# Performance work log

Measured on AMD Instinct MI355X. Metric: run time of the kernel, lower is better.

## Reference

```python
import jax, jax.numpy as jnp
import numpy as np

B, S, D, H, DH, SD = 4, 512, 768, 12, 64, 30
ALPHA, BETA = 1.0, 1.0


def setup_inputs() -> dict:
    root = jax.random.key(0)
    ks = jax.random.split(root, 16)
    n = lambda k, sh: jax.random.normal(k, sh, dtype=jnp.float32)
    w = lambda k, sh: 0.02 * jax.random.normal(k, sh, dtype=jnp.float32)
    return {
        "key": n(ks[0], (B, S, D)),
        "value": n(ks[1], (B, S, D)),
        "query": n(ks[2], (B, S, D)),
        "structure": n(ks[3], (B, S, S, SD)),
        "mask": jax.random.randint(ks[4], (B, S, S), 0, 2).astype(bool),
        "Wq": w(ks[5], (D, D)), "bq": jnp.zeros((D,), jnp.float32),
        "Wk": w(ks[6], (D, D)), "bk": jnp.zeros((D,), jnp.float32),
        "Wv": w(ks[7], (D, D)), "bv": jnp.zeros((D,), jnp.float32),
        "Wsk": w(ks[8], (SD, DH)), "bsk": jnp.zeros((DH,), jnp.float32),
        "Wsv": w(ks[9], (SD, DH)), "bsv": jnp.zeros((DH,), jnp.float32),
        "Wo": w(ks[10], (D, D)), "bo": jnp.zeros((D,), jnp.float32),
    }


def reference(key, value, query, structure, mask,
              Wq, bq, Wk, bk, Wv, bv, Wsk, bsk, Wsv, bsv, Wo, bo):
    # shape: [B,S,D] -> [B,H,S,DH]
    def proj(x, W, b):
        return (x @ W + b).reshape(B, -1, H, DH).transpose(0, 2, 1, 3)

    q = proj(query, Wq, bq) / np.float32(np.sqrt(DH))  # scale applied before both score terms
    k = proj(key, Wk, bk)
    v = proj(value, Wv, bv)

    sk = structure @ Wsk + bsk  # [B,Q,K,DH] relative-structure keys
    sv = structure @ Wsv + bsv  # [B,Q,K,DH] relative-structure values

    scores = jnp.einsum('bhqd,bhkd->bhqk', q, k)
    scores = scores + ALPHA * jnp.einsum('bhqd,bqkd->bhqk', q, sk)
    scores = jnp.where(mask[:, None, :, :], jnp.float32(-1e18), scores)

    attn = jax.nn.softmax(scores, axis=-1)  # dropout p=0 -> identity

    ctx = jnp.einsum('bhqk,bhkd->bhqd', attn, v)
    ctx = ctx + BETA * jnp.einsum('bhqk,bqkd->bhqd', attn, sv)
    ctx = ctx.transpose(0, 2, 1, 3).reshape(B, S, D)

    output = ctx @ Wo + bo
    top_attn = attn[:, 0]  # [B,Q,K]
    return output, top_attn
```

## Files before the change

### kernel.cpp

```cpp
#include <hip/hip_runtime.h>
#include <hip/hip_bf16.h>

typedef unsigned int uint32_ty;

typedef float  nfloat2 __attribute__((ext_vector_type(2)));
typedef float  nfloat4 __attribute__((ext_vector_type(4)));
typedef int    nint4   __attribute__((ext_vector_type(4)));
typedef short  bf16x8  __attribute__((ext_vector_type(8)));
typedef float  f32x4   __attribute__((ext_vector_type(4)));
typedef unsigned short ushort4n __attribute__((ext_vector_type(4)));

#define BB 4
#define SS 512
#define DD 768
#define HH 12
#define DHH 64
#define SDD 30

#define LP 520

__device__ __forceinline__ float bfu(unsigned short u) {
    return __uint_as_float(((uint32_ty)u) << 16);
}
__device__ __forceinline__ unsigned short tobf(float f) {
    return __bfloat16_as_ushort(__float2bfloat16(f));
}
__device__ __forceinline__ void unp8(uint4 u, float* t) {
    t[0] = __uint_as_float(u.x << 16);
    t[1] = __uint_as_float(u.x & 0xFFFF0000u);
    t[2] = __uint_as_float(u.y << 16);
    t[3] = __uint_as_float(u.y & 0xFFFF0000u);
    t[4] = __uint_as_float(u.z << 16);
    t[5] = __uint_as_float(u.z & 0xFFFF0000u);
    t[6] = __uint_as_float(u.w << 16);
    t[7] = __uint_as_float(u.w & 0xFFFF0000u);
}
__device__ __forceinline__ void unp4(uint2 u, float* t) {
    t[0] = __uint_as_float(u.x << 16);
    t[1] = __uint_as_float(u.x & 0xFFFF0000u);
    t[2] = __uint_as_float(u.y << 16);
    t[3] = __uint_as_float(u.y & 0xFFFF0000u);
}

#define MBM 64
#define MBN 64
#define MBK 64
#define LDK 72

__global__ __launch_bounds__(256) void gemm_proj3(
    const float* __restrict__ Xq, const float* __restrict__ Xk, const float* __restrict__ Xv,
    const float* __restrict__ Wq, const float* __restrict__ Wk, const float* __restrict__ Wv,
    const float* __restrict__ bq, const float* __restrict__ bk, const float* __restrict__ bv,
    float* __restrict__ oq, unsigned short* __restrict__ okT, unsigned short* __restrict__ ov)
{
    __shared__ unsigned short As[MBM][LDK];
    __shared__ unsigned short Bs[MBN][LDK];
    int z = blockIdx.z;
    const float* X = (z == 0) ? Xq : (z == 1) ? Xk : Xv;
    const float* W = (z == 0) ? Wq : (z == 1) ? Wk : Wv;
    const float* bias = (z == 0) ? bq : (z == 1) ? bk : bv;

    int tid = threadIdx.x;
    int lane = tid & 63, wave = tid >> 6;
    int m0 = blockIdx.y * MBM, n0 = blockIdx.x * MBN;
    int wm = (wave >> 1) * 32, wn = (wave & 1) * 32;
    int fr = lane & 15, fq = lane >> 4;

    f32x4 acc[2][2];
#pragma unroll
    for (int i = 0; i < 2; i++)
#pragma unroll
        for (int j = 0; j < 2; j++) acc[i][j] = (f32x4){0.f, 0.f, 0.f, 0.f};

    for (int k0 = 0; k0 < DD; k0 += MBK) {
#pragma unroll
        for (int rep = 0; rep < 4; rep++) {
            int i = tid + 256 * rep;
            int r = i >> 4, c4 = i & 15;
            float4 xv = *(const float4*)(X + (size_t)(m0 + r) * DD + k0 + 4 * c4);
            ushort4n pk = {tobf(xv.x), tobf(xv.y), tobf(xv.z), tobf(xv.w)};
            *(ushort4n*)&As[r][4 * c4] = pk;
        }
#pragma unroll
        for (int rep = 0; rep < 4; rep++) {
            int i = tid + 256 * rep;
            int r = i >> 4, c4 = i & 15;
            float4 wv = *(const float4*)(W + (size_t)(k0 + r) * DD + n0 + 4 * c4);
            Bs[4 * c4 + 0][r] = tobf(wv.x);
            Bs[4 * c4 + 1][r] = tobf(wv.y);
            Bs[4 * c4 + 2][r] = tobf(wv.z);
            Bs[4 * c4 + 3][r] = tobf(wv.w);
        }
        __syncthreads();
#pragma unroll
        for (int ks = 0; ks < 2; ks++) {
            bf16x8 a0 = *(bf16x8*)&As[wm + fr][ks * 32 + fq * 8];
            bf16x8 a1 = *(bf16x8*)&As[wm + 16 + fr][ks * 32 + fq * 8];
            bf16x8 b0 = *(bf16x8*)&Bs[wn + fr][ks * 32 + fq * 8];
            bf16x8 b1 = *(bf16x8*)&Bs[wn + 16 + fr][ks * 32 + fq * 8];
            acc[0][0] = __builtin_amdgcn_mfma_f32_16x16x32_bf16(a0, b0, acc[0][0], 0, 0, 0);
            acc[0][1] = __builtin_amdgcn_mfma_f32_16x16x32_bf16(a0, b1, acc[0][1], 0, 0, 0);
            acc[1][0] = __builtin_amdgcn_mfma_f32_16x16x32_bf16(a1, b0, acc[1][0], 0, 0, 0);
            acc[1][1] = __builtin_amdgcn_mfma_f32_16x16x32_bf16(a1, b1, acc[1][1], 0, 0, 0);
        }
        __syncthreads();
    }

#pragma unroll
    for (int i = 0; i < 2; i++) {
#pragma unroll
        for (int j = 0; j < 2; j++) {
            int n = n0 + wn + 16 * j + fr;
            int h = n >> 6, d = n & 63;
            float bn = bias[n];
            int mbase = m0 + wm + 16 * i + fq * 4;
            int b = mbase >> 9, sbase = mbase & 511;
            if (z == 1) {
                ushort4n pk;
#pragma unroll
                for (int r = 0; r < 4; r++) pk[r] = tobf(acc[i][j][r] + bn);
                *(ushort4n*)(okT + ((((size_t)b * HH + h) * DHH + d) * SS + sbase)) = pk;
            } else if (z == 0) {
#pragma unroll
                for (int r = 0; r < 4; r++)
                    oq[((((size_t)b * HH + h) * SS + sbase + r) * DHH + d)] =
                        (acc[i][j][r] + bn) * 0.125f;
            } else {
#pragma unroll
                for (int r = 0; r < 4; r++)
                    ov[((((size_t)b * HH + h) * SS + sbase + r) * DHH + d)] =
                        tobf(acc[i][j][r] + bn);
            }
        }
    }
}

#define TM 64
#define TN 64
#define TKK 32

__global__ __launch_bounds__(256) void gemm_out(
    const float* __restrict__ Xf, const float* __restrict__ W,
    const float* __restrict__ bias, float* __restrict__ out)
{
    __shared__ float As[TKK][TM + 4];
    __shared__ float Bs[TKK][TN + 4];
    int tx = threadIdx.x, ty = threadIdx.y;
    int tid = ty * 16 + tx;
    int m0 = blockIdx.y * TM;
    int n0 = blockIdx.x * TN;
    float acc[4][4] = {};
    for (int k0 = 0; k0 < DD; k0 += TKK) {
#pragma unroll
        for (int rep = 0; rep < 2; rep++) {
            int f = tid + 256 * rep;
            int r = f >> 3, c = f & 7;
            float4 xv = *(const float4*)(Xf + (size_t)(m0 + r) * DD + k0 + 4 * c);
            As[4 * c + 0][r] = xv.x; As[4 * c + 1][r] = xv.y;
            As[4 * c + 2][r] = xv.z; As[4 * c + 3][r] = xv.w;
        }
#pragma unroll
        for (int rep = 0; rep < 2; rep++) {
            int f = tid + 256 * rep;
            int r = f >> 4, c = f & 15;
            float4 wv = *(const float4*)(W + (size_t)(k0 + r) * DD + n0 + 4 * c);
            *(float4*)&Bs[r][4 * c] = wv;
        }
        __syncthreads();
#pragma unroll 8
        for (int kk = 0; kk < TKK; kk++) {
            float4 av = *(float4*)&As[kk][ty * 4];
            float4 bv4 = *(float4*)&Bs[kk][tx * 4];
            float a[4] = {av.x, av.y, av.z, av.w};
            float bb[4] = {bv4.x, bv4.y, bv4.z, bv4.w};
#pragma unroll
            for (int i = 0; i < 4; i++)
#pragma unroll
                for (int j = 0; j < 4; j++) acc[i][j] += a[i] * bb[j];
        }
        __syncthreads();
    }
#pragma unroll
    for (int i = 0; i < 4; i++) {
        int m = m0 + ty * 4 + i;
#pragma unroll
        for (int j = 0; j < 4; j++) {
            int n = n0 + tx * 4 + j;
            out[(size_t)m * DD + n] = acc[i][j] + bias[n];
        }
    }
}

__global__ __launch_bounds__(256) void attn_fused(
    const float* __restrict__ q,
    const unsigned short* __restrict__ kT,
    const unsigned short* __restrict__ v,
    const float* __restrict__ structure,
    const int* __restrict__ mask,
    const float* __restrict__ Wsk,
    const float* __restrict__ bsk,
    const float* __restrict__ Wsv,
    const float* __restrict__ bsv,
    float* __restrict__ ctx,
    float* __restrict__ top_attn)
{
    __shared__ float qs[HH][DHH];
    __shared__ unsigned short stT[SDD][LP];
    __shared__ float qt_s[HH][SDD];
    __shared__ float qb_s[HH];
    __shared__ float astr_s[HH][SDD];
    __shared__ unsigned short at[HH][LP];

    int tid = threadIdx.x;
    int lane = tid & 63, wave = tid >> 6;

    int blk = blockIdx.x;
    int xcd = blk & 7;
    int b = xcd >> 1;
    int qp = ((xcd & 1) << 8) | (blk >> 3);

    for (int i = tid; i < HH * DHH; i += 256) {
        int h = i >> 6, d = i & 63;
        qs[h][d] = q[(((size_t)b * HH + h) * SS + qp) * DHH + d];
    }
    {
        const float* srow = structure + ((size_t)b * SS + qp) * (size_t)(SS * SDD);
        for (int k = tid; k < SS; k += 256) {
            const nfloat2* rp = (const nfloat2*)(srow + (size_t)k * SDD);
#pragma unroll
            for (int w = 0; w < 15; w++) {
                nfloat2 xv = __builtin_nontemporal_load(rp + w);
                stT[2 * w][k] = tobf(xv.x);
                stT[2 * w + 1][k] = tobf(xv.y);
            }
        }
    }
    __syncthreads();

    for (int i = tid; i < HH * SDD; i += 256) {
        int h = i / SDD, si = i % SDD;
        const float4* wp = (const float4*)(Wsk + si * DHH);
        const float4* qp4 = (const float4*)qs[h];
        float a = 0.f;
#pragma unroll
        for (int d4 = 0; d4 < 16; d4++) {
            float4 wv = wp[d4];
            float4 qv = qp4[d4];
            a += qv.x * wv.x + qv.y * wv.y + qv.z * wv.z + qv.w * wv.w;
        }
        qt_s[h][si] = a;
    }
    if (tid < HH) {
        const float4* bp = (const float4*)bsk;
        const float4* qp4 = (const float4*)qs[tid];
        float a = 0.f;
#pragma unroll
        for (int d4 = 0; d4 < 16; d4++) {
            float4 wv = bp[d4];
            float4 qv = qp4[d4];
            a += qv.x * wv.x + qv.y * wv.y + qv.z * wv.z + qv.w * wv.w;
        }
        qb_s[tid] = a;
    }
    __syncthreads();

    int h0 = wave * 3;
    float attnv[3][8];
#pragma unroll
    for (int h = 0; h < 3; h++)
#pragma unroll
        for (int j = 0; j < 8; j++) attnv[h][j] = 0.f;

#pragma unroll 2
    for (int si = 0; si < SDD; si++) {
        uint4 sv4 = *(const uint4*)&stT[si][8 * lane];
        float t[8];
        unp8(sv4, t);
#pragma unroll
        for (int h = 0; h < 3; h++) {
            float qt = qt_s[h0 + h][si];
#pragma unroll
            for (int j = 0; j < 8; j++) attnv[h][j] += qt * t[j];
        }
    }

    {
        const unsigned short* kbase = kT + (((size_t)b * HH + h0) * DHH) * SS + 8 * lane;
#pragma unroll
        for (int h = 0; h < 3; h++) {
            const unsigned short* kp = kbase + (size_t)h * (DHH * SS);
            float acc[8] = {0.f, 0.f, 0.f, 0.f, 0.f, 0.f, 0.f, 0.f};
#pragma unroll 8
            for (int d = 0; d < DHH; d++) {
                float qd = qs[h0 + h][d];
                uint4 kv = *(const uint4*)(kp + (size_t)d * SS);
                float t[8];
                unp8(kv, t);
#pragma unroll
                for (int j = 0; j < 8; j++) acc[j] += qd * t[j];
            }
            float qb = qb_s[h0 + h];
#pragma unroll
            for (int j = 0; j < 8; j++) attnv[h][j] += acc[j] + qb;
        }
    }

    {
        const int* mrow = mask + ((size_t)b * SS + qp) * SS + 8 * lane;
        nint4 m0v = __builtin_nontemporal_load((const nint4*)mrow);
        nint4 m1v = __builtin_nontemporal_load(((const nint4*)mrow) + 1);
        int mm[8] = {m0v.x, m0v.y, m0v.z, m0v.w, m1v.x, m1v.y, m1v.z, m1v.w};
#pragma unroll
        for (int h = 0; h < 3; h++)
#pragma unroll
            for (int j = 0; j < 8; j++)
                if (mm[j]) attnv[h][j] = -1e18f;
    }

#pragma unroll
    for (int h = 0; h < 3; h++) {
        float m = attnv[h][0];
#pragma unroll
        for (int j = 1; j < 8; j++) m = fmaxf(m, attnv[h][j]);
#pragma unroll
        for (int off = 32; off > 0; off >>= 1) m = fmaxf(m, __shfl_xor(m, off));
        float l = 0.f;
#pragma unroll
        for (int j = 0; j < 8; j++) { attnv[h][j] = __expf(attnv[h][j] - m); l += attnv[h][j]; }
#pragma unroll
        for (int off = 32; off > 0; off >>= 1) l += __shfl_xor(l, off);
        float inv = 1.f / l;
        float a[8];
#pragma unroll
        for (int j = 0; j < 8; j++) a[j] = attnv[h][j] * inv;
        uint4 pk;
        pk.x = (uint32_ty)tobf(a[0]) | ((uint32_ty)tobf(a[1]) << 16);
        pk.y = (uint32_ty)tobf(a[2]) | ((uint32_ty)tobf(a[3]) << 16);
        pk.z = (uint32_ty)tobf(a[4]) | ((uint32_ty)tobf(a[5]) << 16);
        pk.w = (uint32_ty)tobf(a[6]) | ((uint32_ty)tobf(a[7]) << 16);
        *(uint4*)&at[h0 + h][8 * lane] = pk;
        if (h0 + h == 0) {
            float* tp = top_attn + ((size_t)b * SS + qp) * SS + 8 * lane;
            nfloat4 w0 = {a[0], a[1], a[2], a[3]};
            nfloat4 w1 = {a[4], a[5], a[6], a[7]};
            __builtin_nontemporal_store(w0, (nfloat4*)tp);
            __builtin_nontemporal_store(w1, ((nfloat4*)tp) + 1);
        }
    }
    __syncthreads();

    if (tid < 180) {
        int h = tid / 15, sp = tid % 15;
        int si0 = 2 * sp, si1 = si0 + 1;
        float a0e = 0.f, a0o = 0.f, a1e = 0.f, a1o = 0.f;
#pragma unroll 2
        for (int j = 0; j < 64; j++) {
            uint4 av = *(const uint4*)&at[h][8 * j];
            uint4 s0 = *(const uint4*)&stT[si0][8 * j];
            uint4 s1 = *(const uint4*)&stT[si1][8 * j];
            float a[8], t0[8], t1[8];
            unp8(av, a); unp8(s0, t0); unp8(s1, t1);
#pragma unroll
            for (int t = 0; t < 8; t += 2) {
                a0e += a[t] * t0[t];     a0o += a[t + 1] * t0[t + 1];
                a1e += a[t] * t1[t];     a1o += a[t + 1] * t1[t + 1];
            }
        }
        astr_s[h][si0] = a0e + a0o;
        astr_s[h][si1] = a1e + a1o;
    }
    __syncthreads();

    if (tid < 192) {
        int h = tid >> 4, dq = tid & 15;
        const unsigned short* vp = v + ((size_t)b * HH + h) * (size_t)(SS * DHH) + 4 * dq;
        float4 ae; ae.x = ae.y = ae.z = ae.w = 0.f;
        float4 ao; ao.x = ao.y = ao.z = ao.w = 0.f;
#pragma unroll 2
        for (int j = 0; j < 64; j++) {
            uint4 av = *(const uint4*)&at[h][8 * j];
            float a[8];
            unp8(av, a);
            const unsigned short* vk = vp + (size_t)(8 * j) * DHH;
#pragma unroll
            for (int t = 0; t < 8; t += 2) {
                uint2 v0 = *(const uint2*)(vk + (size_t)t * DHH);
                uint2 v1 = *(const uint2*)(vk + (size_t)(t + 1) * DHH);
                float f0[4], f1[4];
                unp4(v0, f0); unp4(v1, f1);
                ae.x += a[t] * f0[0]; ae.y += a[t] * f0[1];
                ae.z += a[t] * f0[2]; ae.w += a[t] * f0[3];
                ao.x += a[t + 1] * f1[0]; ao.y += a[t + 1] * f1[1];
                ao.z += a[t + 1] * f1[2]; ao.w += a[t + 1] * f1[3];
            }
        }
        float4 sa = *(const float4*)(bsv + 4 * dq);
#pragma unroll
        for (int si = 0; si < SDD; si++) {
            float as = astr_s[h][si];
            float4 wv = *(const float4*)(Wsv + si * DHH + 4 * dq);
            sa.x += as * wv.x; sa.y += as * wv.y;
            sa.z += as * wv.z; sa.w += as * wv.w;
        }
        float4 outv;
        outv.x = ae.x + ao.x + sa.x;
        outv.y = ae.y + ao.y + sa.y;
        outv.z = ae.z + ao.z + sa.z;
        outv.w = ae.w + ao.w + sa.w;
        *(float4*)(ctx + ((size_t)b * SS + qp) * DD + h * DHH + 4 * dq) = outv;
    }
}

extern "C" void kernel_launch(void* const* d_in, const int* in_sizes, int n_in,
                              void* d_out, int out_size, void* d_ws, size_t ws_size,
                              hipStream_t stream)
{
    const float* key       = (const float*)d_in[0];
    const float* value     = (const float*)d_in[1];
    const float* query     = (const float*)d_in[2];
    const float* structure = (const float*)d_in[3];
    const int*   mask      = (const int*)d_in[4];
    const float* Wq  = (const float*)d_in[5];
    const float* bq  = (const float*)d_in[6];
    const float* Wk  = (const float*)d_in[7];
    const float* bk  = (const float*)d_in[8];
    const float* Wv  = (const float*)d_in[9];
    const float* bv  = (const float*)d_in[10];
    const float* Wsk = (const float*)d_in[11];
    const float* bsk = (const float*)d_in[12];
    const float* Wsv = (const float*)d_in[13];
    const float* bsv = (const float*)d_in[14];
    const float* Wo  = (const float*)d_in[15];
    const float* bo  = (const float*)d_in[16];

    float* out_main = (float*)d_out;
    float* out_attn = (float*)d_out + (size_t)BB * SS * DD;

    float* ws = (float*)d_ws;
    float*          q_buf   = ws;
    unsigned short* kT_buf  = (unsigned short*)(ws + 1572864);
    unsigned short* v_buf   = (unsigned short*)(ws + 2359296);
    float*          ctx_buf = ws + 3145728;

    dim3 ggrd3(DD / MBN, (BB * SS) / MBM, 3);
    gemm_proj3<<<ggrd3, dim3(256), 0, stream>>>(query, key, value, Wq, Wk, Wv,
                                                bq, bk, bv, q_buf, kT_buf, v_buf);

    attn_fused<<<BB * SS, 256, 0, stream>>>(q_buf, kT_buf, v_buf, structure, mask,
                                            Wsk, bsk, Wsv, bsv, ctx_buf, out_attn);

    dim3 ggrd(DD / TN, (BB * SS) / TM);
    gemm_out<<<ggrd, dim3(16, 16), 0, stream>>>(ctx_buf, Wo, bo, out_main);
}
```

Before: 521.4 us.

## Switch intermediates to fp16 and use packed dot2 for score and context

Measured after the change: 859.6 us. 1.65x slower.

```diff
diff --git a/kernel.cpp b/kernel.cpp
--- a/kernel.cpp
+++ b/kernel.cpp
@@ -1,13 +1,14 @@
 #include <hip/hip_runtime.h>
-#include <hip/hip_bf16.h>
+#include <hip/hip_fp16.h>
 
 typedef unsigned int uint32_ty;
 
-typedef float  nfloat2 __attribute__((ext_vector_type(2)));
-typedef float  nfloat4 __attribute__((ext_vector_type(4)));
-typedef int    nint4   __attribute__((ext_vector_type(4)));
-typedef short  bf16x8  __attribute__((ext_vector_type(8)));
-typedef float  f32x4   __attribute__((ext_vector_type(4)));
+typedef float    nfloat2 __attribute__((ext_vector_type(2)));
+typedef float    nfloat4 __attribute__((ext_vector_type(4)));
+typedef int      nint4   __attribute__((ext_vector_type(4)));
+typedef _Float16 h16x2   __attribute__((ext_vector_type(2)));
+typedef _Float16 f16x8   __attribute__((ext_vector_type(8)));
+typedef float    f32x4   __attribute__((ext_vector_type(4)));
 typedef unsigned short ushort4n __attribute__((ext_vector_type(4)));
 
 #define BB 4
@@ -19,27 +20,28 @@
 
 #define LP 520
 
-__device__ __forceinline__ float bfu(unsigned short u) {
-    return __uint_as_float(((uint32_ty)u) << 16);
-}
-__device__ __forceinline__ unsigned short tobf(float f) {
-    return __bfloat16_as_ushort(__float2bfloat16(f));
-}
-__device__ __forceinline__ void unp8(uint4 u, float* t) {
-    t[0] = __uint_as_float(u.x << 16);
-    t[1] = __uint_as_float(u.x & 0xFFFF0000u);
-    t[2] = __uint_as_float(u.y << 16);
-    t[3] = __uint_as_float(u.y & 0xFFFF0000u);
-    t[4] = __uint_as_float(u.z << 16);
-    t[5] = __uint_as_float(u.z & 0xFFFF0000u);
-    t[6] = __uint_as_float(u.w << 16);
-    t[7] = __uint_as_float(u.w & 0xFFFF0000u);
-}
-__device__ __forceinline__ void unp4(uint2 u, float* t) {
-    t[0] = __uint_as_float(u.x << 16);
-    t[1] = __uint_as_float(u.x & 0xFFFF0000u);
-    t[2] = __uint_as_float(u.y << 16);
-    t[3] = __uint_as_float(u.y & 0xFFFF0000u);
+__device__ __forceinline__ unsigned short toh(float f) {
+    _Float16 h = (_Float16)f;
+    return __builtin_bit_cast(unsigned short, h);
+}
+__device__ __forceinline__ float hf(unsigned short u) {
+    return (float)__builtin_bit_cast(_Float16, u);
+}
+__device__ __forceinline__ float dot2(uint32_ty a, uint32_ty b, float c) {
+#if __has_builtin(__builtin_amdgcn_fdot2)
+    return __builtin_amdgcn_fdot2(__builtin_bit_cast(h16x2, a),
+                                  __builtin_bit_cast(h16x2, b), c, false);
+#else
+    h16x2 x = __builtin_bit_cast(h16x2, a), y = __builtin_bit_cast(h16x2, b);
+    return c + (float)x.x * (float)y.x + (float)x.y * (float)y.y;
+#endif
+}
+__device__ __forceinline__ void unp8h(uint4 u, float* t) {
+    h16x2 p;
+    p = __builtin_bit_cast(h16x2, u.x); t[0] = p.x; t[1] = p.y;
+    p = __builtin_bit_cast(h16x2, u.y); t[2] = p.x; t[3] = p.y;
+    p = __builtin_bit_cast(h16x2, u.z); t[4] = p.x; t[5] = p.y;
+    p = __builtin_bit_cast(h16x2, u.w); t[6] = p.x; t[7] = p.y;
 }
 
 #define MBM 64
@@ -51,7 +53,8 @@
     const float* __restrict__ Xq, const float* __restrict__ Xk, const float* __restrict__ Xv,
     const float* __restrict__ Wq, const float* __restrict__ Wk, const float* __restrict__ Wv,
     const float* __restrict__ bq, const float* __restrict__ bk, const float* __restrict__ bv,
-    float* __restrict__ oq, unsigned short* __restrict__ okT, unsigned short* __restrict__ ov)
+    unsigned short* __restrict__ oq, unsigned short* __restrict__ ok,
+    unsigned short* __restrict__ ovT)
 {
     __shared__ unsigned short As[MBM][LDK];
     __shared__ unsigned short Bs[MBN][LDK];
@@ -78,7 +81,7 @@
             int i = tid + 256 * rep;
             int r = i >> 4, c4 = i & 15;
             float4 xv = *(const float4*)(X + (size_t)(m0 + r) * DD + k0 + 4 * c4);
-            ushort4n pk = {tobf(xv.x), tobf(xv.y), tobf(xv.z), tobf(xv.w)};
+            ushort4n pk = {toh(xv.x), toh(xv.y), toh(xv.z), toh(xv.w)};
             *(ushort4n*)&As[r][4 * c4] = pk;
         }
 #pragma unroll
@@ -86,22 +89,22 @@
             int i = tid + 256 * rep;
             int r = i >> 4, c4 = i & 15;
             float4 wv = *(const float4*)(W + (size_t)(k0 + r) * DD + n0 + 4 * c4);
-            Bs[4 * c4 + 0][r] = tobf(wv.x);
-            Bs[4 * c4 + 1][r] = tobf(wv.y);
-            Bs[4 * c4 + 2][r] = tobf(wv.z);
-            Bs[4 * c4 + 3][r] = tobf(wv.w);
+            Bs[4 * c4 + 0][r] = toh(wv.x);
+            Bs[4 * c4 + 1][r] = toh(wv.y);
+            Bs[4 * c4 + 2][r] = toh(wv.z);
+            Bs[4 * c4 + 3][r] = toh(wv.w);
         }
         __syncthreads();
 #pragma unroll
         for (int ks = 0; ks < 2; ks++) {
-            bf16x8 a0 = *(bf16x8*)&As[wm + fr][ks * 32 + fq * 8];
-            bf16x8 a1 = *(bf16x8*)&As[wm + 16 + fr][ks * 32 + fq * 8];
-            bf16x8 b0 = *(bf16x8*)&Bs[wn + fr][ks * 32 + fq * 8];
-            bf16x8 b1 = *(bf16x8*)&Bs[wn + 16 + fr][ks * 32 + fq * 8];
-            acc[0][0] = __builtin_amdgcn_mfma_f32_16x16x32_bf16(a0, b0, acc[0][0], 0, 0, 0);
-            acc[0][1] = __builtin_amdgcn_mfma_f32_16x16x32_bf16(a0, b1, acc[0][1], 0, 0, 0);
-            acc[1][0] = __builtin_amdgcn_mfma_f32_16x16x32_bf16(a1, b0, acc[1][0], 0, 0, 0);
-            acc[1][1] = __builtin_amdgcn_mfma_f32_16x16x32_bf16(a1, b1, acc[1][1], 0, 0, 0);
+            f16x8 a0 = *(f16x8*)&As[wm + fr][ks * 32 + fq * 8];
+            f16x8 a1 = *(f16x8*)&As[wm + 16 + fr][ks * 32 + fq * 8];
+            f16x8 b0 = *(f16x8*)&Bs[wn + fr][ks * 32 + fq * 8];
+            f16x8 b1 = *(f16x8*)&Bs[wn + 16 + fr][ks * 32 + fq * 8];
+            acc[0][0] = __builtin_amdgcn_mfma_f32_16x16x32_f16(a0, b0, acc[0][0], 0, 0, 0);
+            acc[0][1] = __builtin_amdgcn_mfma_f32_16x16x32_f16(a0, b1, acc[0][1], 0, 0, 0);
+            acc[1][0] = __builtin_amdgcn_mfma_f32_16x16x32_f16(a1, b0, acc[1][0], 0, 0, 0);
+            acc[1][1] = __builtin_amdgcn_mfma_f32_16x16x32_f16(a1, b1, acc[1][1], 0, 0, 0);
         }
         __syncthreads();
     }
@@ -115,21 +118,21 @@
             float bn = bias[n];
             int mbase = m0 + wm + 16 * i + fq * 4;
             int b = mbase >> 9, sbase = mbase & 511;
-            if (z == 1) {
+            if (z == 2) {
                 ushort4n pk;
 #pragma unroll
-                for (int r = 0; r < 4; r++) pk[r] = tobf(acc[i][j][r] + bn);
-                *(ushort4n*)(okT + ((((size_t)b * HH + h) * DHH + d) * SS + sbase)) = pk;
+                for (int r = 0; r < 4; r++) pk[r] = toh(acc[i][j][r] + bn);
+                *(ushort4n*)(ovT + ((((size_t)b * HH + h) * DHH + d) * SS + sbase)) = pk;
             } else if (z == 0) {
 #pragma unroll
                 for (int r = 0; r < 4; r++)
                     oq[((((size_t)b * HH + h) * SS + sbase + r) * DHH + d)] =
-                        (acc[i][j][r] + bn) * 0.125f;
+                        toh((acc[i][j][r] + bn) * 0.125f);
             } else {
 #pragma unroll
                 for (int r = 0; r < 4; r++)
-                    ov[((((size_t)b * HH + h) * SS + sbase + r) * DHH + d)] =
-                        tobf(acc[i][j][r] + bn);
+                    ok[((((size_t)b * HH + h) * SS + sbase + r) * DHH + d)] =
+                        toh(acc[i][j][r] + bn);
             }
         }
     }
@@ -192,9 +195,9 @@
 }
 
 __global__ __launch_bounds__(256) void attn_fused(
-    const float* __restrict__ q,
-    const unsigned short* __restrict__ kT,
-    const unsigned short* __restrict__ v,
+    const unsigned short* __restrict__ q,
+    const unsigned short* __restrict__ k,
+    const unsigned short* __restrict__ vT,
     const float* __restrict__ structure,
     const int* __restrict__ mask,
     const float* __restrict__ Wsk,
@@ -204,7 +207,7 @@
     float* __restrict__ ctx,
     float* __restrict__ top_attn)
 {
-    __shared__ float qs[HH][DHH];
+    __shared__ uint32_ty qs32[HH * 32];
     __shared__ unsigned short stT[SDD][LP];
     __shared__ float qt_s[HH][SDD];
     __shared__ float qb_s[HH];
@@ -219,19 +222,19 @@
     int b = xcd >> 1;
     int qp = ((xcd & 1) << 8) | (blk >> 3);
 
-    for (int i = tid; i < HH * DHH; i += 256) {
-        int h = i >> 6, d = i & 63;
-        qs[h][d] = q[(((size_t)b * HH + h) * SS + qp) * DHH + d];
+    for (int i = tid; i < HH * 32; i += 256) {
+        int h = i >> 5, c = i & 31;
+        qs32[i] = *(const uint32_ty*)(q + (((size_t)b * HH + h) * SS + qp) * DHH + 2 * c);
     }
     {
         const float* srow = structure + ((size_t)b * SS + qp) * (size_t)(SS * SDD);
-        for (int k = tid; k < SS; k += 256) {
-            const nfloat2* rp = (const nfloat2*)(srow + (size_t)k * SDD);
+        for (int kk = tid; kk < SS; kk += 256) {
+            const nfloat2* rp = (const nfloat2*)(srow + (size_t)kk * SDD);
 #pragma unroll
             for (int w = 0; w < 15; w++) {
                 nfloat2 xv = __builtin_nontemporal_load(rp + w);
-                stT[2 * w][k] = tobf(xv.x);
-                stT[2 * w + 1][k] = tobf(xv.y);
+                stT[2 * w][kk] = toh(xv.x);
+                stT[2 * w + 1][kk] = toh(xv.y);
             }
         }
     }
@@ -239,26 +242,23 @@
 
     for (int i = tid; i < HH * SDD; i += 256) {
         int h = i / SDD, si = i % SDD;
-        const float4* wp = (const float4*)(Wsk + si * DHH);
-        const float4* qp4 = (const float4*)qs[h];
+        const uint32_ty* qp32 = &qs32[h * 32];
+        const float* wp = Wsk + si * DHH;
         float a = 0.f;
 #pragma unroll
-        for (int d4 = 0; d4 < 16; d4++) {
-            float4 wv = wp[d4];
-            float4 qv = qp4[d4];
-            a += qv.x * wv.x + qv.y * wv.y + qv.z * wv.z + qv.w * wv.w;
+        for (int c = 0; c < 32; c++) {
+            h16x2 p = __builtin_bit_cast(h16x2, qp32[c]);
+            a += (float)p.x * wp[2 * c] + (float)p.y * wp[2 * c + 1];
         }
         qt_s[h][si] = a;
     }
     if (tid < HH) {
-        const float4* bp = (const float4*)bsk;
-        const float4* qp4 = (const float4*)qs[tid];
+        const uint32_ty* qp32 = &qs32[tid * 32];
         float a = 0.f;
 #pragma unroll
-        for (int d4 = 0; d4 < 16; d4++) {
-            float4 wv = bp[d4];
-            float4 qv = qp4[d4];
-            a += qv.x * wv.x + qv.y * wv.y + qv.z * wv.z + qv.w * wv.w;
+        for (int c = 0; c < 32; c++) {
+            h16x2 p = __builtin_bit_cast(h16x2, qp32[c]);
+            a += (float)p.x * bsk[2 * c] + (float)p.y * bsk[2 * c + 1];
         }
         qb_s[tid] = a;
     }
@@ -275,7 +275,7 @@
     for (int si = 0; si < SDD; si++) {
         uint4 sv4 = *(const uint4*)&stT[si][8 * lane];
         float t[8];
-        unp8(sv4, t);
+        unp8h(sv4, t);
 #pragma unroll
         for (int h = 0; h < 3; h++) {
             float qt = qt_s[h0 + h][si];
@@ -284,24 +284,27 @@
         }
     }
 
-    {
-        const unsigned short* kbase = kT + (((size_t)b * HH + h0) * DHH) * SS + 8 * lane;
-#pragma unroll
-        for (int h = 0; h < 3; h++) {
-            const unsigned short* kp = kbase + (size_t)h * (DHH * SS);
-            float acc[8] = {0.f, 0.f, 0.f, 0.f, 0.f, 0.f, 0.f, 0.f};
-#pragma unroll 8
-            for (int d = 0; d < DHH; d++) {
-                float qd = qs[h0 + h][d];
-                uint4 kv = *(const uint4*)(kp + (size_t)d * SS);
-                float t[8];
-                unp8(kv, t);
-#pragma unroll
-                for (int j = 0; j < 8; j++) acc[j] += qd * t[j];
+#pragma unroll
+    for (int h = 0; h < 3; h++) {
+        const unsigned short* kh = k + (size_t)((size_t)b * HH + h0 + h) * SS * DHH;
+        const uint4* qp4 = (const uint4*)&qs32[(h0 + h) * 32];
+        uint4 qr[8];
+#pragma unroll
+        for (int c = 0; c < 8; c++) qr[c] = qp4[c];
+        float qb = qb_s[h0 + h];
+#pragma unroll
+        for (int j = 0; j < 8; j++) {
+            const uint4* kr = (const uint4*)(kh + (size_t)(8 * lane + j) * DHH);
+            float s0 = 0.f, s1 = 0.f, s2 = 0.f, s3 = 0.f;
+#pragma unroll
+            for (int c = 0; c < 8; c++) {
+                uint4 kv = kr[c];
+                s0 = dot2(qr[c].x, kv.x, s0);
+                s1 = dot2(qr[c].y, kv.y, s1);
+                s2 = dot2(qr[c].z, kv.z, s2);
+                s3 = dot2(qr[c].w, kv.w, s3);
             }
-            float qb = qb_s[h0 + h];
-#pragma unroll
-            for (int j = 0; j < 8; j++) attnv[h][j] += acc[j] + qb;
+            attnv[h][j] += s0 + s1 + s2 + s3 + qb;
         }
     }
 
@@ -334,10 +337,10 @@
 #pragma unroll
         for (int j = 0; j < 8; j++) a[j] = attnv[h][j] * inv;
         uint4 pk;
-        pk.x = (uint32_ty)tobf(a[0]) | ((uint32_ty)tobf(a[1]) << 16);
-        pk.y = (uint32_ty)tobf(a[2]) | ((uint32_ty)tobf(a[3]) << 16);
-        pk.z = (uint32_ty)tobf(a[4]) | ((uint32_ty)tobf(a[5]) << 16);
-        pk.w = (uint32_ty)tobf(a[6]) | ((uint32_ty)tobf(a[7]) << 16);
+        pk.x = (uint32_ty)toh(a[0]) | ((uint32_ty)toh(a[1]) << 16);
+        pk.y = (uint32_ty)toh(a[2]) | ((uint32_ty)toh(a[3]) << 16);
+        pk.z = (uint32_ty)toh(a[4]) | ((uint32_ty)toh(a[5]) << 16);
+        pk.w = (uint32_ty)toh(a[6]) | ((uint32_ty)toh(a[7]) << 16);
         *(uint4*)&at[h0 + h][8 * lane] = pk;
         if (h0 + h == 0) {
             float* tp = top_attn + ((size_t)b * SS + qp) * SS + 8 * lane;
@@ -352,62 +355,41 @@
     if (tid < 180) {
         int h = tid / 15, sp = tid % 15;
         int si0 = 2 * sp, si1 = si0 + 1;
-        float a0e = 0.f, a0o = 0.f, a1e = 0.f, a1o = 0.f;
-#pragma unroll 2
+        float a0 = 0.f, b0 = 0.f, a1 = 0.f, b1 = 0.f;
+#pragma unroll 4
         for (int j = 0; j < 64; j++) {
             uint4 av = *(const uint4*)&at[h][8 * j];
             uint4 s0 = *(const uint4*)&stT[si0][8 * j];
             uint4 s1 = *(const uint4*)&stT[si1][8 * j];
-            float a[8], t0[8], t1[8];
-            unp8(av, a); unp8(s0, t0); unp8(s1, t1);
-#pragma unroll
-            for (int t = 0; t < 8; t += 2) {
-                a0e += a[t] * t0[t];     a0o += a[t + 1] * t0[t + 1];
-                a1e += a[t] * t1[t];     a1o += a[t + 1] * t1[t + 1];
-            }
-        }
-        astr_s[h][si0] = a0e + a0o;
-        astr_s[h][si1] = a1e + a1o;
+            a0 = dot2(av.x, s0.x, a0); b0 = dot2(av.y, s0.y, b0);
+            a0 = dot2(av.z, s0.z, a0); b0 = dot2(av.w, s0.w, b0);
+            a1 = dot2(av.x, s1.x, a1); b1 = dot2(av.y, s1.y, b1);
+            a1 = dot2(av.z, s1.z, a1); b1 = dot2(av.w, s1.w, b1);
+        }
+        astr_s[h][si0] = a0 + b0;
+        astr_s[h][si1] = a1 + b1;
     }
     __syncthreads();
 
-    if (tid < 192) {
-        int h = tid >> 4, dq = tid & 15;
-        const unsigned short* vp = v + ((size_t)b * HH + h) * (size_t)(SS * DHH) + 4 * dq;
-        float4 ae; ae.x = ae.y = ae.z = ae.w = 0.f;
-        float4 ao; ao.x = ao.y = ao.z = ao.w = 0.f;
-#pragma unroll 2
+#pragma unroll
+    for (int r = 0; r < 3; r++) {
+        int o = tid + 256 * r;
+        int h = o >> 6, d = o & 63;
+        const uint4* vr = (const uint4*)(vT + (((size_t)b * HH + h) * DHH + d) * SS);
+        float s0 = 0.f, s1 = 0.f, s2 = 0.f, s3 = 0.f;
+#pragma unroll 4
         for (int j = 0; j < 64; j++) {
             uint4 av = *(const uint4*)&at[h][8 * j];
-            float a[8];
-            unp8(av, a);
-            const unsigned short* vk = vp + (size_t)(8 * j) * DHH;
-#pragma unroll
-            for (int t = 0; t < 8; t += 2) {
-                uint2 v0 = *(const uint2*)(vk + (size_t)t * DHH);
-                uint2 v1 = *(const uint2*)(vk + (size_t)(t + 1) * DHH);
-                float f0[4], f1[4];
-                unp4(v0, f0); unp4(v1, f1);
-                ae.x += a[t] * f0[0]; ae.y += a[t] * f0[1];
-                ae.z += a[t] * f0[2]; ae.w += a[t] * f0[3];
-                ao.x += a[t + 1] * f1[0]; ao.y += a[t + 1] * f1[1];
-                ao.z += a[t + 1] * f1[2]; ao.w += a[t + 1] * f1[3];
-            }
-        }
-        float4 sa = *(const float4*)(bsv + 4 * dq);
-#pragma unroll
-        for (int si = 0; si < SDD; si++) {
-            float as = astr_s[h][si];
-            float4 wv = *(const float4*)(Wsv + si * DHH + 4 * dq);
-            sa.x += as * wv.x; sa.y += as * wv.y;
-            sa.z += as * wv.z; sa.w += as * wv.w;
-        }
-        float4 outv;
-        outv.x = ae.x + ao.x + sa.x;
-        outv.y = ae.y + ao.y + sa.y;
-        outv.z = ae.z + ao.z + sa.z;
-        outv.w = ae.w + ao.w + sa.w;
-        *(float4*)(ctx + ((size_t)b * SS + qp) * DD + h * DHH + 4 * dq) = outv;
+            uint4 vv = vr[j];
+            s0 = dot2(av.x, vv.x, s0);
+            s1 = dot2(av.y, vv.y, s1);
+            s2 = dot2(av.z, vv.z, s2);
+            s3 = dot2(av.w, vv.w, s3);
+        }
+        float sa = bsv[d];
+#pragma unroll
+        for (int si = 0; si < SDD; si++) sa += astr_s[h][si] * Wsv[si * DHH + d];
+        ctx[((size_t)b * SS + qp) * DD + o] = s0 + s1 + s2 + s3 + sa;
     }
 }
 
@@ -437,16 +419,16 @@
     float* out_attn = (float*)d_out + (size_t)BB * SS * DD;
 
     float* ws = (float*)d_ws;
-    float*          q_buf   = ws;
-    unsigned short* kT_buf  = (unsigned short*)(ws + 1572864);
-    unsigned short* v_buf   = (unsigned short*)(ws + 2359296);
-    float*          ctx_buf = ws + 3145728;
+    unsigned short* q_buf  = (unsigned short*)ws;
+    unsigned short* k_buf  = (unsigned short*)(ws + 786432);
+    unsigned short* vT_buf = (unsigned short*)(ws + 1572864);
+    float*          ctx_buf = ws + 2359296;
 
     dim3 ggrd3(DD / MBN, (BB * SS) / MBM, 3);
     gemm_proj3<<<ggrd3, dim3(256), 0, stream>>>(query, key, value, Wq, Wk, Wv,
-                                                bq, bk, bv, q_buf, kT_buf, v_buf);
-
-    attn_fused<<<BB * SS, 256, 0, stream>>>(q_buf, kT_buf, v_buf, structure, mask,
+                                                bq, bk, bv, q_buf, k_buf, vT_buf);
+
+    attn_fused<<<BB * SS, 256, 0, stream>>>(q_buf, k_buf, vT_buf, structure, mask,
                                             Wsk, bsk, Wsv, bsv, ctx_buf, out_attn);
 
     dim3 ggrd(DD / TN, (BB * SS) / TM);
```
